# Kernel tuning notes

Hardware: AMD Instinct MI355X
Metric: run time of the kernel (lower is better)

Reference implementation:

```python
import jax, jax.numpy as jnp
import numpy as np


def setup_inputs() -> dict:
    key = jax.random.key(0)
    k1, k2 = jax.random.split(key)
    B, N, D, F = 4, 50000, 64, 100000
    verts = jax.random.normal(k1, (B, N, D), dtype=jnp.float32)
    faces = jax.random.randint(k2, (B, F, 3), 0, N, dtype=jnp.int64)
    return {"verts": verts, "faces": faces}


def reference(verts, faces):
    # verts: [B, N, D], faces: [B, F, L] int indices into N
    B, N, D = verts.shape
    Ldeg = faces.shape[-1]
    # flatten batch into one block-diagonal graph, as the torch module does
    offset = (jnp.arange(B, dtype=faces.dtype) * N)[:, None, None]
    f = (faces + offset).reshape(-1, Ldeg)          # [B*F, L]
    row = f.reshape(-1)                              # f[:, 0..L-1]
    col = jnp.roll(f, -1, axis=1).reshape(-1)        # f[:, 1..L-1, 0]
    # L = L + L.T -> edges in both directions (duplicates accumulate)
    src = jnp.concatenate([row, col])
    dst = jnp.concatenate([col, row])
    Vf = verts.reshape(-1, D)                        # [B*N, D]
    # off-diagonal: -sum_j V_j over incident half-edges (with multiplicity)
    neigh = jax.ops.segment_sum(Vf[dst], src, num_segments=B * N)
    # Lii = degree (count of incident half-edges)
    deg = jax.ops.segment_sum(jnp.ones_like(src, dtype=verts.dtype), src,
                              num_segments=B * N)    # [B*N]
    # x = (Lii * V_i - sum_j V_j) / (Lii + eps)
    x = (deg[:, None] * Vf - neigh) / (deg[:, None] + 1e-12)
    return x.reshape(B, N, D)
```

## Files before the change

### kernel.cpp

```cpp
#include <hip/hip_runtime.h>
#include <hip/hip_fp16.h>

constexpr int Bc = 4;
constexpr int Nc = 50000;
constexpr int Dc = 64;
constexpr int Fc = 100000;
constexpr int BN = Bc * Nc;
constexpr int NFACES = Bc * Fc;
constexpr int NINC = NFACES * 3;
constexpr int CAP_E = 31;

constexpr int BINV_SH = 9;
constexpr int NBINS   = (BN + 511) / 512;
constexpr int BINCAP  = 4096;
constexpr int BIN3B   = 256;
constexpr int FPB     = (NFACES + BIN3B - 1) / BIN3B;
constexpr int CONVB   = (BN * Dc / 8) / 256;

constexpr size_t A_VH    = 0;
constexpr size_t A_REC   = 25600000;
constexpr size_t A_ENT   = 51200000;
constexpr size_t A_BCUR  = A_ENT + (size_t)NBINS * BINCAP * 8;
constexpr size_t A2_NEED = A_BCUR + (size_t)NBINS * 32 * 4;
constexpr size_t A_NEED  = 51200000;

__global__ __launch_bounds__(256) void bin_conv(
        const float* __restrict__ verts,
        const int*   __restrict__ faces,
        __half* __restrict__ vh,
        int*   __restrict__ bincur,
        uint2* __restrict__ entries) {
    __shared__ unsigned int sfaces[FPB * 3];
    __shared__ int scnt[NBINS];
    __shared__ int sbase[NBINS];

    if ((int)blockIdx.x < BIN3B) {
        int blk = blockIdx.x, t = threadIdx.x;
        int f0g = blk * FPB;
        int nf  = NFACES - f0g; if (nf > FPB) nf = FPB;

        for (int i = t; i < nf * 3; i += 256) sfaces[i] = (unsigned int)faces[f0g * 3 + i];
        for (int i = t; i < NBINS; i += 256) scnt[i] = 0;
        __syncthreads();

        for (int f = t; f < nf; f += 256) {
            int base = ((f0g + f) / Fc) * Nc;
            int g0 = (int)sfaces[3*f+0] + base;
            int g1 = (int)sfaces[3*f+1] + base;
            int g2 = (int)sfaces[3*f+2] + base;
            atomicAdd(&scnt[g0 >> BINV_SH], 1);
            atomicAdd(&scnt[g1 >> BINV_SH], 1);
            atomicAdd(&scnt[g2 >> BINV_SH], 1);
        }
        __syncthreads();

        for (int i = t; i < NBINS; i += 256) {
            int c = scnt[i];
            sbase[i] = (c > 0) ? atomicAdd(&bincur[i * 32], c) : 0;
            scnt[i] = 0;
        }
        __syncthreads();

        for (int f = t; f < nf; f += 256) {
            unsigned int u0 = sfaces[3*f+0];
            unsigned int u1 = sfaces[3*f+1];
            unsigned int u2 = sfaces[3*f+2];
            int base = ((f0g + f) / Fc) * Nc;
            int g0 = (int)u0 + base, g1 = (int)u1 + base, g2 = (int)u2 + base;
            int b0 = g0 >> BINV_SH, b1 = g1 >> BINV_SH, b2 = g2 >> BINV_SH;
            int p0 = sbase[b0] + atomicAdd(&scnt[b0], 1);
            if (p0 < BINCAP) entries[(size_t)b0 * BINCAP + p0] = make_uint2((unsigned)g0, u1 | (u2 << 16));
            int p1 = sbase[b1] + atomicAdd(&scnt[b1], 1);
            if (p1 < BINCAP) entries[(size_t)b1 * BINCAP + p1] = make_uint2((unsigned)g1, u0 | (u2 << 16));
            int p2 = sbase[b2] + atomicAdd(&scnt[b2], 1);
            if (p2 < BINCAP) entries[(size_t)b2 * BINCAP + p2] = make_uint2((unsigned)g2, u0 | (u1 << 16));
        }
    } else {
        long idx = ((long)(blockIdx.x - BIN3B) * 256 + threadIdx.x) * 8;
        float4 a = *(const float4*)(verts + idx);
        float4 b = *(const float4*)(verts + idx + 4);
        __half h[8];
        h[0] = __float2half(a.x); h[1] = __float2half(a.y);
        h[2] = __float2half(a.z); h[3] = __float2half(a.w);
        h[4] = __float2half(b.x); h[5] = __float2half(b.y);
        h[6] = __float2half(b.z); h[7] = __float2half(b.w);
        *(uint4*)(vh + idx) = *(const uint4*)h;
    }
}

__global__ __launch_bounds__(256) void bucket_fill(
        const uint2* __restrict__ entries,
        const int*   __restrict__ bincur,
        unsigned int* __restrict__ rec) {
    __shared__ unsigned int scnt[512];
    __shared__ unsigned int sent[512 * 31];

    int bin = blockIdx.x, t = threadIdx.x;
    for (int i = t; i < 512; i += 256) scnt[i] = 0;
    __syncthreads();

    int total = bincur[bin * 32];
    if (total > BINCAP) total = BINCAP;
    const uint2* e = entries + (size_t)bin * BINCAP;
    for (int i = t; i < total; i += 256) {
        uint2 en = e[i];
        int vl = (int)en.x - (bin << BINV_SH);
        unsigned int r = atomicAdd(&scnt[vl], 1);
        if (r < (unsigned)CAP_E) sent[vl * 31 + r] = en.y;
    }
    __syncthreads();

    int nrec = BN - (bin << BINV_SH); if (nrec > 512) nrec = 512;
    int limit = nrec * 32;
    unsigned int* dst = rec + (size_t)bin * (512 * 32);
    for (int g = t * 4; g < limit; g += 1024) {
        int vl = g >> 5, w = g & 31;
        uint4 u;
        u.x = (w == 0) ? scnt[vl] : sent[vl * 31 + (w - 1)];
        u.y = sent[vl * 31 + w];
        u.z = sent[vl * 31 + w + 1];
        u.w = sent[vl * 31 + w + 2];
        *(uint4*)(dst + g) = u;
    }
}

__global__ __launch_bounds__(256) void conv_fill(
        const float* __restrict__ verts,
        const int*   __restrict__ faces,
        __half* __restrict__ vh,
        unsigned int* __restrict__ rec) {
    constexpr int FILLB = (NFACES + 255) / 256;
    if ((int)blockIdx.x < FILLB) {
        int f = blockIdx.x * 256 + threadIdx.x;
        if (f >= NFACES) return;
        int base = (f / Fc) * Nc;
        unsigned int u0 = (unsigned int)faces[3*f+0];
        unsigned int u1 = (unsigned int)faces[3*f+1];
        unsigned int u2 = (unsigned int)faces[3*f+2];
        unsigned int* r0 = rec + (long)((int)u0 + base) * 32;
        unsigned int* r1 = rec + (long)((int)u1 + base) * 32;
        unsigned int* r2 = rec + (long)((int)u2 + base) * 32;
        int s0 = atomicAdd((int*)r0, 1);
        if (s0 < CAP_E) r0[1 + s0] = u1 | (u2 << 16);
        int s1 = atomicAdd((int*)r1, 1);
        if (s1 < CAP_E) r1[1 + s1] = u0 | (u2 << 16);
        int s2 = atomicAdd((int*)r2, 1);
        if (s2 < CAP_E) r2[1 + s2] = u0 | (u1 << 16);
    } else {
        long idx = ((long)(blockIdx.x - FILLB) * 256 + threadIdx.x) * 8;
        float4 a = *(const float4*)(verts + idx);
        float4 b = *(const float4*)(verts + idx + 4);
        __half h[8];
        h[0] = __float2half(a.x); h[1] = __float2half(a.y);
        h[2] = __float2half(a.z); h[3] = __float2half(a.w);
        h[4] = __float2half(b.x); h[5] = __float2half(b.y);
        h[6] = __float2half(b.z); h[7] = __float2half(b.w);
        *(uint4*)(vh + idx) = *(const uint4*)h;
    }
}

__global__ __launch_bounds__(256) void gather2(
        const float*  __restrict__ verts,
        const __half* __restrict__ vh,
        const unsigned int* __restrict__ rec,
        float* __restrict__ out) {
    int gtid = blockIdx.x * 256 + threadIdx.x;
    int w    = gtid >> 6;
    int lane = threadIdx.x & 63;
    int half = lane >> 5;
    int j    = lane & 31;
    int v    = 2 * w + half;
    int h32  = half << 5;

    unsigned int rw = rec[(long)w * 64 + lane];
    int c = __shfl((int)rw, h32);
    if (c > CAP_E) c = CAP_E;
    int cother = __shfl(c, lane ^ 32);
    int cmax = c > cother ? c : cother;

    int base = (v / Nc) * Nc;
    const __half2* vh2 = (const __half2*)vh;

    float2 own = ((const float2*)verts)[(long)v * 32 + j];

    float accx = 0.f, accy = 0.f;
    for (int i = 0; i < cmax; i += 4) {
        int s1 = i + 2 < 31 ? i + 2 : 31;
        int s2 = i + 3 < 31 ? i + 3 : 31;
        int s3 = i + 4 < 31 ? i + 4 : 31;
        unsigned int p0 = (unsigned int)__shfl((int)rw, h32 + i + 1);
        unsigned int p1 = (unsigned int)__shfl((int)rw, h32 + s1);
        unsigned int p2 = (unsigned int)__shfl((int)rw, h32 + s2);
        unsigned int p3 = (unsigned int)__shfl((int)rw, h32 + s3);
        float m0 = (i     < c) ? 1.f : 0.f;
        float m1 = (i + 1 < c) ? 1.f : 0.f;
        float m2 = (i + 2 < c) ? 1.f : 0.f;
        float m3 = (i + 3 < c) ? 1.f : 0.f;
        unsigned int q0 = (i     < c) ? p0 : 0u;
        unsigned int q1 = (i + 1 < c) ? p1 : 0u;
        unsigned int q2 = (i + 2 < c) ? p2 : 0u;
        unsigned int q3 = (i + 3 < c) ? p3 : 0u;
        long r0 = (long)(base + (int)(q0 & 0xFFFFu)) * 32 + j;
        long r1 = (long)(base + (int)(q0 >> 16))     * 32 + j;
        long r2 = (long)(base + (int)(q1 & 0xFFFFu)) * 32 + j;
        long r3 = (long)(base + (int)(q1 >> 16))     * 32 + j;
        long r4 = (long)(base + (int)(q2 & 0xFFFFu)) * 32 + j;
        long r5 = (long)(base + (int)(q2 >> 16))     * 32 + j;
        long r6 = (long)(base + (int)(q3 & 0xFFFFu)) * 32 + j;
        long r7 = (long)(base + (int)(q3 >> 16))     * 32 + j;
        float2 f0 = __half22float2(vh2[r0]);
        float2 f1 = __half22float2(vh2[r1]);
        float2 f2 = __half22float2(vh2[r2]);
        float2 f3 = __half22float2(vh2[r3]);
        float2 f4 = __half22float2(vh2[r4]);
        float2 f5 = __half22float2(vh2[r5]);
        float2 f6 = __half22float2(vh2[r6]);
        float2 f7 = __half22float2(vh2[r7]);
        accx += m0 * (f0.x + f1.x) + m1 * (f2.x + f3.x)
              + m2 * (f4.x + f5.x) + m3 * (f6.x + f7.x);
        accy += m0 * (f0.y + f1.y) + m1 * (f2.y + f3.y)
              + m2 * (f4.y + f5.y) + m3 * (f6.y + f7.y);
    }

    float deg = 2.0f * (float)c;
    float den = deg + 1e-12f;
    float2 r;
    r.x = (deg * own.x - accx) / den;
    r.y = (deg * own.y - accy) / den;
    ((float2*)out)[(long)v * 32 + j] = r;
}

constexpr int SCAN_ELEMS = 1024;
constexpr int NSCAN = (BN + SCAN_ELEMS - 1) / SCAN_ELEMS;
constexpr size_t WS_COUNTS  = 0;
constexpr size_t WS_OFFSETS = 800000;
constexpr size_t WS_CURSORS = 1600000;
constexpr size_t WS_BSUMS   = 2400000;
constexpr size_t WS_BBASE   = 2401024;
constexpr size_t WS_ENTRIES = 2402048;
constexpr size_t WS_NEEDED  = WS_ENTRIES + (size_t)NINC * 8;

__global__ __launch_bounds__(256) void count_kernel(
        const int* __restrict__ faces, int* __restrict__ counts) {
    int f = blockIdx.x * blockDim.x + threadIdx.x;
    if (f >= NFACES) return;
    int base = (f / Fc) * Nc;
    atomicAdd(&counts[faces[3*f+0] + base], 1);
    atomicAdd(&counts[faces[3*f+1] + base], 1);
    atomicAdd(&counts[faces[3*f+2] + base], 1);
}

__global__ __launch_bounds__(256) void scanA(
        const int* __restrict__ counts, int* __restrict__ bsums) {
    __shared__ int s[256];
    int t = threadIdx.x, b = blockIdx.x;
    int idx = b * SCAN_ELEMS + t * 4;
    int v = 0;
    if (idx + 4 <= BN) {
        int4 c = *(const int4*)(counts + idx);
        v = c.x + c.y + c.z + c.w;
    }
    s[t] = v; __syncthreads();
    for (int o = 128; o > 0; o >>= 1) {
        if (t < o) s[t] += s[t + o];
        __syncthreads();
    }
    if (t == 0) bsums[b] = s[0];
}

__global__ __launch_bounds__(256) void scanB(
        const int* __restrict__ bsums, int* __restrict__ bbase) {
    __shared__ int s[256];
    int t = threadIdx.x;
    int x = (t < NSCAN) ? bsums[t] : 0;
    s[t] = x; __syncthreads();
    for (int o = 1; o < 256; o <<= 1) {
        int v = (t >= o) ? s[t - o] : 0;
        __syncthreads();
        s[t] += v;
        __syncthreads();
    }
    bbase[t] = s[t] - x;
}

__global__ __launch_bounds__(256) void scanC(
        const int* __restrict__ counts, const int* __restrict__ bbase,
        int* __restrict__ offsets) {
    __shared__ int s[256];
    int t = threadIdx.x, b = blockIdx.x;
    int idx = b * SCAN_ELEMS + t * 4;
    int4 c = make_int4(0, 0, 0, 0);
    bool ok = (idx + 4 <= BN);
    if (ok) c = *(const int4*)(counts + idx);
    int tsum = c.x + c.y + c.z + c.w;
    s[t] = tsum; __syncthreads();
    for (int o = 1; o < 256; o <<= 1) {
        int v = (t >= o) ? s[t - o] : 0;
        __syncthreads();
        s[t] += v;
        __syncthreads();
    }
    int tbase = bbase[b] + s[t] - tsum;
    if (ok) {
        int4 o4;
        o4.x = tbase;
        o4.y = tbase + c.x;
        o4.z = tbase + c.x + c.y;
        o4.w = tbase + c.x + c.y + c.z;
        *(int4*)(offsets + idx) = o4;
    }
}

__global__ __launch_bounds__(256) void fill_kernel(
        const int* __restrict__ faces,
        const int* __restrict__ offsets,
        int* __restrict__ cursors,
        int2* __restrict__ entries) {
    int f = blockIdx.x * blockDim.x + threadIdx.x;
    if (f >= NFACES) return;
    int base = (f / Fc) * Nc;
    int v0 = faces[3*f+0] + base;
    int v1 = faces[3*f+1] + base;
    int v2 = faces[3*f+2] + base;
    int p0 = offsets[v0] + atomicAdd(&cursors[v0], 1);
    entries[p0] = make_int2(v1, v2);
    int p1 = offsets[v1] + atomicAdd(&cursors[v1], 1);
    entries[p1] = make_int2(v0, v2);
    int p2 = offsets[v2] + atomicAdd(&cursors[v2], 1);
    entries[p2] = make_int2(v0, v1);
}

__global__ __launch_bounds__(256) void gather_kernel(
        const float* __restrict__ verts,
        const int* __restrict__ counts,
        const int* __restrict__ offsets,
        const int2* __restrict__ entries,
        float* __restrict__ out) {
    int v    = (int)((blockIdx.x * blockDim.x + threadIdx.x) >> 6);
    int lane = threadIdx.x & 63;
    if (v >= BN) return;
    int c = counts[v];
    const int2* e = entries + offsets[v];
    float acc = 0.f;
    int i = 0;
    for (; i + 2 <= c; i += 2) {
        int2 a = e[i];
        int2 b = e[i + 1];
        acc += verts[(long)a.x * Dc + lane] + verts[(long)a.y * Dc + lane]
             + verts[(long)b.x * Dc + lane] + verts[(long)b.y * Dc + lane];
    }
    if (i < c) {
        int2 a = e[i];
        acc += verts[(long)a.x * Dc + lane] + verts[(long)a.y * Dc + lane];
    }
    float deg = 2.0f * (float)c;
    float own = verts[(long)v * Dc + lane];
    out[(long)v * Dc + lane] = (deg * own - acc) / (deg + 1e-12f);
}

extern "C" void kernel_launch(void* const* d_in, const int* in_sizes, int n_in,
                              void* d_out, int out_size, void* d_ws, size_t ws_size,
                              hipStream_t stream) {
    const float* verts = (const float*)d_in[0];
    const int*   faces = (const int*)d_in[1];
    float* out = (float*)d_out;
    char*  ws  = (char*)d_ws;

    if (ws_size >= A2_NEED) {
        __half*       vh      = (__half*)(ws + A_VH);
        unsigned int* rec     = (unsigned int*)(ws + A_REC);
        uint2*        entries = (uint2*)(ws + A_ENT);
        int*          bincur  = (int*)(ws + A_BCUR);

        hipMemsetAsync(bincur, 0, (size_t)NBINS * 32 * sizeof(int), stream);
        bin_conv<<<BIN3B + CONVB, 256, 0, stream>>>(verts, faces, vh, bincur, entries);
        bucket_fill<<<NBINS, 256, 0, stream>>>(entries, bincur, rec);
        gather2<<<BN * 32 / 256, 256, 0, stream>>>(verts, vh, rec, out);
    } else if (ws_size >= A_NEED) {
        __half*       vh  = (__half*)(ws + A_VH);
        unsigned int* rec = (unsigned int*)(ws + A_REC);
        hipMemsetAsync(rec, 0, (size_t)BN * 32 * sizeof(unsigned int), stream);
        conv_fill<<<(NFACES + 255) / 256 + CONVB, 256, 0, stream>>>(verts, faces, vh, rec);
        gather2<<<BN * 32 / 256, 256, 0, stream>>>(verts, vh, rec, out);
    } else if (ws_size >= WS_NEEDED) {
        int*  counts  = (int*)(ws + WS_COUNTS);
        int*  offsets = (int*)(ws + WS_OFFSETS);
        int*  cursors = (int*)(ws + WS_CURSORS);
        int*  bsums   = (int*)(ws + WS_BSUMS);
        int*  bbase   = (int*)(ws + WS_BBASE);
        int2* entries = (int2*)(ws + WS_ENTRIES);

        hipMemsetAsync(counts,  0, (size_t)BN * sizeof(int), stream);
        hipMemsetAsync(cursors, 0, (size_t)BN * sizeof(int), stream);
        int fb = (NFACES + 255) / 256;
        count_kernel<<<fb, 256, 0, stream>>>(faces, counts);
        scanA<<<NSCAN, 256, 0, stream>>>(counts, bsums);
        scanB<<<1, 256, 0, stream>>>(bsums, bbase);
        scanC<<<NSCAN, 256, 0, stream>>>(counts, bbase, offsets);
        fill_kernel<<<fb, 256, 0, stream>>>(faces, offsets, cursors, entries);
        int gb = (BN * 64 + 255) / 256;
        gather_kernel<<<gb, 256, 0, stream>>>(verts, counts, offsets, entries, out);
    }
}
```

Measured before the change: 168.2 us.

## Fuse bucket fill into gather, using per-batch zero sentinel rows in fp16 verts

The separate bucket_fill pass, which wrote per-vertex neighbour records to global memory, is merged with the gather into one kernel. Each block now owns 256 vertices, builds the neighbour lists in shared memory, then gathers the fp16 neighbour features directly. This removes the global record write and read-back and one kernel launch. The fp16 vertex copy is padded with a zero row per batch, so unused slots point at that row and the gather needs no masking. The own-vertex term now comes from the fp16 copy instead of fp32 verts, which loses some precision, and only 64 KB of blocks per 256 vertices gives fewer waves per block to hide gather latency.

```diff
diff --git a/kernel.cpp b/kernel.cpp
--- a/kernel.cpp
+++ b/kernel.cpp
@@ -10,19 +10,18 @@
 constexpr int NINC = NFACES * 3;
 constexpr int CAP_E = 31;
 
-constexpr int BINV_SH = 9;
-constexpr int NBINS   = (BN + 511) / 512;
-constexpr int BINCAP  = 4096;
+constexpr int BINV_SH = 8;
+constexpr int NBINS   = (BN + 255) / 256;
+constexpr int BINCAP  = 2048;
 constexpr int BIN3B   = 256;
 constexpr int FPB     = (NFACES + BIN3B - 1) / BIN3B;
 constexpr int CONVB   = (BN * Dc / 8) / 256;
+constexpr unsigned int SENT = (unsigned)Nc | ((unsigned)Nc << 16);
 
 constexpr size_t A_VH    = 0;
-constexpr size_t A_REC   = 25600000;
-constexpr size_t A_ENT   = 51200000;
+constexpr size_t A_ENT   = 25600512;
 constexpr size_t A_BCUR  = A_ENT + (size_t)NBINS * BINCAP * 8;
-constexpr size_t A2_NEED = A_BCUR + (size_t)NBINS * 32 * 4;
-constexpr size_t A_NEED  = 51200000;
+constexpr size_t A3_NEED = A_BCUR + (size_t)NBINS * 32 * 4;
 
 __global__ __launch_bounds__(256) void bin_conv(
         const float* __restrict__ verts,
@@ -75,54 +74,107 @@
             int p2 = sbase[b2] + atomicAdd(&scnt[b2], 1);
             if (p2 < BINCAP) entries[(size_t)b2 * BINCAP + p2] = make_uint2((unsigned)g2, u0 | (u1 << 16));
         }
+    } else if ((int)blockIdx.x < BIN3B + CONVB) {
+        long idx = ((long)(blockIdx.x - BIN3B) * 256 + threadIdx.x) * 8;
+        int  v   = (int)(idx >> 6);
+        int  b   = v / Nc;
+        float4 a = *(const float4*)(verts + idx);
+        float4 bb = *(const float4*)(verts + idx + 4);
+        __half h[8];
+        h[0] = __float2half(a.x);  h[1] = __float2half(a.y);
+        h[2] = __float2half(a.z);  h[3] = __float2half(a.w);
+        h[4] = __float2half(bb.x); h[5] = __float2half(bb.y);
+        h[6] = __float2half(bb.z); h[7] = __float2half(bb.w);
+        *(uint4*)(vh + idx + (long)b * 64) = *(const uint4*)h;
     } else {
-        long idx = ((long)(blockIdx.x - BIN3B) * 256 + threadIdx.x) * 8;
-        float4 a = *(const float4*)(verts + idx);
-        float4 b = *(const float4*)(verts + idx + 4);
-        __half h[8];
-        h[0] = __float2half(a.x); h[1] = __float2half(a.y);
-        h[2] = __float2half(a.z); h[3] = __float2half(a.w);
-        h[4] = __float2half(b.x); h[5] = __float2half(b.y);
-        h[6] = __float2half(b.z); h[7] = __float2half(b.w);
-        *(uint4*)(vh + idx) = *(const uint4*)h;
-    }
-}
-
-__global__ __launch_bounds__(256) void bucket_fill(
-        const uint2* __restrict__ entries,
-        const int*   __restrict__ bincur,
-        unsigned int* __restrict__ rec) {
-    __shared__ unsigned int scnt[512];
-    __shared__ unsigned int sent[512 * 31];
+        int t = threadIdx.x;
+        if (t < 128) {
+            int b = t >> 5, w = t & 31;
+            ((unsigned int*)vh)[(long)(b * (Nc + 1) + Nc) * 32 + w] = 0u;
+        }
+    }
+}
+
+__global__ __launch_bounds__(256) void bucket_gather(
+        const __half* __restrict__ vh,
+        const uint2*  __restrict__ entries,
+        const int*    __restrict__ bincur,
+        float* __restrict__ out) {
+    __shared__ unsigned int scnt[256];
+    __shared__ unsigned int sent[256 * 32];
 
     int bin = blockIdx.x, t = threadIdx.x;
-    for (int i = t; i < 512; i += 256) scnt[i] = 0;
+    scnt[t] = 0;
+    for (int i = t; i < 256 * 32; i += 256) sent[i] = SENT;
     __syncthreads();
 
     int total = bincur[bin * 32];
     if (total > BINCAP) total = BINCAP;
     const uint2* e = entries + (size_t)bin * BINCAP;
+    int v0 = bin << BINV_SH;
     for (int i = t; i < total; i += 256) {
         uint2 en = e[i];
-        int vl = (int)en.x - (bin << BINV_SH);
+        int vl = (int)en.x - v0;
         unsigned int r = atomicAdd(&scnt[vl], 1);
-        if (r < (unsigned)CAP_E) sent[vl * 31 + r] = en.y;
+        if (r < (unsigned)CAP_E) sent[(vl << 5) + r] = en.y;
     }
     __syncthreads();
 
-    int nrec = BN - (bin << BINV_SH); if (nrec > 512) nrec = 512;
-    int limit = nrec * 32;
-    unsigned int* dst = rec + (size_t)bin * (512 * 32);
-    for (int g = t * 4; g < limit; g += 1024) {
-        int vl = g >> 5, w = g & 31;
-        uint4 u;
-        u.x = (w == 0) ? scnt[vl] : sent[vl * 31 + (w - 1)];
-        u.y = sent[vl * 31 + w];
-        u.z = sent[vl * 31 + w + 1];
-        u.w = sent[vl * 31 + w + 2];
-        *(uint4*)(dst + g) = u;
-    }
-}
+    int lane = t & 63, wv = t >> 6;
+    int half = lane >> 5, j = lane & 31;
+    const __half2* vh2 = (const __half2*)vh;
+    int nrec = BN - v0; if (nrec > 256) nrec = 256;
+
+    for (int pair = wv; pair * 2 < nrec; pair += 4) {
+        int vl = pair * 2 + half;
+        int v  = v0 + vl;
+        int c  = (int)scnt[vl]; if (c > CAP_E) c = CAP_E;
+        int cother = __shfl(c, lane ^ 32);
+        int cmax = c > cother ? c : cother;
+        int b = v / Nc;
+        int base2 = b * (Nc + 1);
+
+        float2 own = __half22float2(vh2[(v + b) * 32 + j]);
+
+        const unsigned int* se = &sent[vl << 5];
+        float accx = 0.f, accy = 0.f;
+        for (int i = 0; i < cmax; i += 4) {
+            unsigned int p0 = se[i];
+            unsigned int p1 = se[i + 1];
+            unsigned int p2 = se[i + 2];
+            unsigned int p3 = se[i + 3];
+            int r0 = (base2 + (int)(p0 & 0xFFFFu)) * 32 + j;
+            int r1 = (base2 + (int)(p0 >> 16))     * 32 + j;
+            int r2 = (base2 + (int)(p1 & 0xFFFFu)) * 32 + j;
+            int r3 = (base2 + (int)(p1 >> 16))     * 32 + j;
+            int r4 = (base2 + (int)(p2 & 0xFFFFu)) * 32 + j;
+            int r5 = (base2 + (int)(p2 >> 16))     * 32 + j;
+            int r6 = (base2 + (int)(p3 & 0xFFFFu)) * 32 + j;
+            int r7 = (base2 + (int)(p3 >> 16))     * 32 + j;
+            float2 f0 = __half22float2(vh2[r0]);
+            float2 f1 = __half22float2(vh2[r1]);
+            float2 f2 = __half22float2(vh2[r2]);
+            float2 f3 = __half22float2(vh2[r3]);
+            float2 f4 = __half22float2(vh2[r4]);
+            float2 f5 = __half22float2(vh2[r5]);
+            float2 f6 = __half22float2(vh2[r6]);
+            float2 f7 = __half22float2(vh2[r7]);
+            accx += (f0.x + f1.x) + (f2.x + f3.x) + (f4.x + f5.x) + (f6.x + f7.x);
+            accy += (f0.y + f1.y) + (f2.y + f3.y) + (f4.y + f5.y) + (f6.y + f7.y);
+        }
+
+        float deg = 2.0f * (float)c;
+        float den = deg + 1e-12f;
+        float2 r;
+        r.x = (deg * own.x - accx) / den;
+        r.y = (deg * own.y - accy) / den;
+        ((float2*)out)[(long)v * 32 + j] = r;
+    }
+}
+
+constexpr size_t B_VH   = 0;
+constexpr size_t B_REC  = 25600000;
+constexpr size_t B_NEED = 51200000;
 
 __global__ __launch_bounds__(256) void conv_fill(
         const float* __restrict__ verts,
@@ -180,46 +232,26 @@
 
     int base = (v / Nc) * Nc;
     const __half2* vh2 = (const __half2*)vh;
-
     float2 own = ((const float2*)verts)[(long)v * 32 + j];
 
     float accx = 0.f, accy = 0.f;
-    for (int i = 0; i < cmax; i += 4) {
-        int s1 = i + 2 < 31 ? i + 2 : 31;
-        int s2 = i + 3 < 31 ? i + 3 : 31;
-        int s3 = i + 4 < 31 ? i + 4 : 31;
-        unsigned int p0 = (unsigned int)__shfl((int)rw, h32 + i + 1);
-        unsigned int p1 = (unsigned int)__shfl((int)rw, h32 + s1);
-        unsigned int p2 = (unsigned int)__shfl((int)rw, h32 + s2);
-        unsigned int p3 = (unsigned int)__shfl((int)rw, h32 + s3);
-        float m0 = (i     < c) ? 1.f : 0.f;
+    for (int i = 0; i < cmax; i += 2) {
+        unsigned int p0 = (unsigned int)__shfl((int)rw, h32 + 1 + i);
+        unsigned int p1 = (unsigned int)__shfl((int)rw, h32 + 2 + i);
+        float m0 = (i < c) ? 1.f : 0.f;
         float m1 = (i + 1 < c) ? 1.f : 0.f;
-        float m2 = (i + 2 < c) ? 1.f : 0.f;
-        float m3 = (i + 3 < c) ? 1.f : 0.f;
-        unsigned int q0 = (i     < c) ? p0 : 0u;
+        unsigned int q0 = (i < c) ? p0 : 0u;
         unsigned int q1 = (i + 1 < c) ? p1 : 0u;
-        unsigned int q2 = (i + 2 < c) ? p2 : 0u;
-        unsigned int q3 = (i + 3 < c) ? p3 : 0u;
         long r0 = (long)(base + (int)(q0 & 0xFFFFu)) * 32 + j;
         long r1 = (long)(base + (int)(q0 >> 16))     * 32 + j;
         long r2 = (long)(base + (int)(q1 & 0xFFFFu)) * 32 + j;
         long r3 = (long)(base + (int)(q1 >> 16))     * 32 + j;
-        long r4 = (long)(base + (int)(q2 & 0xFFFFu)) * 32 + j;
-        long r5 = (long)(base + (int)(q2 >> 16))     * 32 + j;
-        long r6 = (long)(base + (int)(q3 & 0xFFFFu)) * 32 + j;
-        long r7 = (long)(base + (int)(q3 >> 16))     * 32 + j;
         float2 f0 = __half22float2(vh2[r0]);
         float2 f1 = __half22float2(vh2[r1]);
         float2 f2 = __half22float2(vh2[r2]);
         float2 f3 = __half22float2(vh2[r3]);
-        float2 f4 = __half22float2(vh2[r4]);
-        float2 f5 = __half22float2(vh2[r5]);
-        float2 f6 = __half22float2(vh2[r6]);
-        float2 f7 = __half22float2(vh2[r7]);
-        accx += m0 * (f0.x + f1.x) + m1 * (f2.x + f3.x)
-              + m2 * (f4.x + f5.x) + m3 * (f6.x + f7.x);
-        accy += m0 * (f0.y + f1.y) + m1 * (f2.y + f3.y)
-              + m2 * (f4.y + f5.y) + m3 * (f6.y + f7.y);
+        accx += m0 * (f0.x + f1.x) + m1 * (f2.x + f3.x);
+        accy += m0 * (f0.y + f1.y) + m1 * (f2.y + f3.y);
     }
 
     float deg = 2.0f * (float)c;
@@ -366,19 +398,17 @@
     float* out = (float*)d_out;
     char*  ws  = (char*)d_ws;
 
-    if (ws_size >= A2_NEED) {
+    if (ws_size >= A3_NEED) {
         __half*       vh      = (__half*)(ws + A_VH);
-        unsigned int* rec     = (unsigned int*)(ws + A_REC);
         uint2*        entries = (uint2*)(ws + A_ENT);
         int*          bincur  = (int*)(ws + A_BCUR);
 
         hipMemsetAsync(bincur, 0, (size_t)NBINS * 32 * sizeof(int), stream);
-        bin_conv<<<BIN3B + CONVB, 256, 0, stream>>>(verts, faces, vh, bincur, entries);
-        bucket_fill<<<NBINS, 256, 0, stream>>>(entries, bincur, rec);
-        gather2<<<BN * 32 / 256, 256, 0, stream>>>(verts, vh, rec, out);
-    } else if (ws_size >= A_NEED) {
-        __half*       vh  = (__half*)(ws + A_VH);
-        unsigned int* rec = (unsigned int*)(ws + A_REC);
+        bin_conv<<<BIN3B + CONVB + 1, 256, 0, stream>>>(verts, faces, vh, bincur, entries);
+        bucket_gather<<<NBINS, 256, 0, stream>>>(vh, entries, bincur, out);
+    } else if (ws_size >= B_NEED) {
+        __half*       vh  = (__half*)(ws + B_VH);
+        unsigned int* rec = (unsigned int*)(ws + B_REC);
         hipMemsetAsync(rec, 0, (size_t)BN * 32 * sizeof(unsigned int), stream);
         conv_fill<<<(NFACES + 255) / 256 + CONVB, 256, 0, stream>>>(verts, faces, vh, rec);
         gather2<<<BN * 32 / 256, 256, 0, stream>>>(verts, vh, rec, out);
```

Result: no change. 167.9 us (-0.2%).
